# Kernel optimization log

Hardware: AMD Instinct MI355X
Metric: run time of the kernel (lower is better)

## Reference

```python
import jax, jax.numpy as jnp
from jax import lax
import numpy as np

N_POINTS = 2_000_000
EXTENT = 512          # fine voxel extent per axis
STRIDE = 16           # pool kernel/stride
G = EXTENT // STRIDE  # coarse grid per axis = 32
C_IN = 3
C_OUT = 64
K = 3                 # conv kernel size


def setup_inputs() -> dict:
    key = jax.random.key(0)
    k1, k2, k3 = jax.random.split(key, 3)
    coords = jax.random.randint(k1, (N_POINTS, 3), 0, EXTENT, dtype=jnp.int32)
    feats = jax.random.normal(k2, (N_POINTS, C_IN), dtype=jnp.float32)
    # MinkowskiConvolution kernel (no bias by default): [out, in, kD, kH, kW]
    fan_in = C_IN * K ** 3
    W = jax.random.normal(k3, (C_OUT, C_IN, K, K, K), dtype=jnp.float32) / np.sqrt(fan_in)
    return {"coords": coords, "feats": feats, "W": W}


def reference(coords, feats, W):
    # --- MinkowskiAvgPooling(kernel=16, stride=16) ---
    # coarse voxel id per point; average of features of occupied fine voxels in block
    cid = coords // STRIDE                               # [N,3] in [0,G)
    idx = (cid[:, 0] * G + cid[:, 1]) * G + cid[:, 2]    # [N] linearized coarse id
    n_seg = G * G * G
    sums = jax.ops.segment_sum(feats, idx, num_segments=n_seg)               # [G^3,Cin]
    cnt = jax.ops.segment_sum(jnp.ones((feats.shape[0], 1), feats.dtype), idx,
                              num_segments=n_seg)                            # [G^3,1]
    avg = sums / jnp.maximum(cnt, 1.0)                   # zeros at empty coarse voxels

    # --- MinkowskiConvolution(Cin->Cout, k=3, stride=1) on coarse sparse grid ---
    # Empty neighbors contribute zero features, so a dense SAME conv over the
    # zero-filled coarse grid matches the sparse kernel-map gather.
    grid = avg.reshape(1, G, G, G, C_IN).transpose(0, 4, 1, 2, 3)   # NCDHW
    conv = lax.conv_general_dilated(
        grid, W, window_strides=(1, 1, 1), padding="SAME",
        dimension_numbers=("NCDHW", "OIDHW", "NCDHW"))               # [1,Cout,G,G,G]
    # conv outputs only at occupied coarse coords (Minkowski semantics)
    occ = (cnt > 0).astype(conv.dtype).reshape(1, 1, G, G, G)
    conv = conv * occ

    # --- MinkowskiPoolingTranspose(kernel=16, stride=16) ---
    # broadcast each coarse feature back to the occupied fine coords in its block
    flat = conv.transpose(0, 2, 3, 4, 1).reshape(n_seg, C_OUT)       # [G^3,Cout]
    out = flat[idx]                                                  # [N,Cout]
    return out
```

## Files before the change

### kernel.cpp

```cpp
#include <hip/hip_runtime.h>

#define G 32
#define NCELL (G * G * G)
#define C_IN 3
#define C_OUT 64
#define PBLK 64
#define HTHREADS 1024

typedef float f32x4 __attribute__((ext_vector_type(4)));
typedef int   i32x4 __attribute__((ext_vector_type(4)));


__global__ void cellid_kernel(const i32x4* __restrict__ coords4,
                              int* __restrict__ cellid, int n) {
    int t = blockIdx.x * blockDim.x + threadIdx.x;
    int base = t * 4;
    if (base >= n) return;
    i32x4 a = coords4[t * 3 + 0];
    i32x4 b = coords4[t * 3 + 1];
    i32x4 c = coords4[t * 3 + 2];
    int c0 = (((a.x >> 4) * G + (a.y >> 4)) * G + (a.z >> 4));
    int c1 = (((a.w >> 4) * G + (b.x >> 4)) * G + (b.y >> 4));
    int c2 = (((b.z >> 4) * G + (b.w >> 4)) * G + (c.x >> 4));
    int c3 = (((c.y >> 4) * G + (c.z >> 4)) * G + (c.w >> 4));
    if (base + 3 < n) {
        i32x4 r = {c0, c1, c2, c3};
        *(i32x4*)&cellid[base] = r;
    } else {
        cellid[base] = c0;
        if (base + 1 < n) cellid[base + 1] = c1;
        if (base + 2 < n) cellid[base + 2] = c2;
    }
}

__global__ __launch_bounds__(HTHREADS) void histo_kernel(
    const int* __restrict__ cellid,
    const float* __restrict__ feats,
    float* __restrict__ partial,
    int n, int ppc) {
    __shared__ __align__(16) float h[NCELL];
    int vtype = blockIdx.x & 3;
    int chunk = blockIdx.x >> 2;

    f32x4* h4 = (f32x4*)h;
    for (int t = threadIdx.x; t < NCELL / 4; t += HTHREADS)
        h4[t] = (f32x4){0.f, 0.f, 0.f, 0.f};
    __syncthreads();

    int start = chunk * ppc;
    int end = start + ppc; if (end > n) end = n;
    if (vtype < 3) {
        for (int i = start + threadIdx.x; i < end; i += HTHREADS) {
            int c = cellid[i];
            atomicAdd(&h[c], feats[i * 3 + vtype]);
        }
    } else {
        for (int i = start + threadIdx.x; i < end; i += HTHREADS) {
            int c = cellid[i];
            atomicAdd(&h[c], 1.0f);
        }
    }
    __syncthreads();

    f32x4* pp = (f32x4*)(partial + ((size_t)vtype * PBLK + chunk) * NCELL);
    for (int t = threadIdx.x; t < NCELL / 4; t += HTHREADS)
        pp[t] = h4[t];
}

__global__ void reduce_kernel(const float* __restrict__ partial,
                              float* __restrict__ avg) {
    int cell = blockIdx.x * blockDim.x + threadIdx.x;
    if (cell >= NCELL) return;
    float s0 = 0.f, s1 = 0.f, s2 = 0.f, c = 0.f;
    for (int p = 0; p < PBLK; ++p) {
        s0 += partial[((size_t)0 * PBLK + p) * NCELL + cell];
        s1 += partial[((size_t)1 * PBLK + p) * NCELL + cell];
        s2 += partial[((size_t)2 * PBLK + p) * NCELL + cell];
        c  += partial[((size_t)3 * PBLK + p) * NCELL + cell];
    }
    float inv = c > 0.f ? 1.0f / c : 0.f;
    avg[cell * 3 + 0] = s0 * inv;
    avg[cell * 3 + 1] = s1 * inv;
    avg[cell * 3 + 2] = s2 * inv;
}

__global__ void conv_kernel(const float* __restrict__ avg,
                            const float* __restrict__ W,
                            float* __restrict__ convout) {
    __shared__ float wlds[C_OUT * C_IN * 27];
    for (int t = threadIdx.x; t < C_OUT * C_IN * 27; t += blockDim.x)
        wlds[t] = W[t];
    __syncthreads();

    int cell = blockIdx.x * blockDim.x + threadIdx.x;
    if (cell >= NCELL) return;
    int z = cell & 31;
    int y = (cell >> 5) & 31;
    int x = cell >> 10;

    float acc[C_OUT];
#pragma unroll
    for (int c = 0; c < C_OUT; ++c) acc[c] = 0.f;

    for (int kd = 0; kd < 3; ++kd) {
        int nx = x + kd - 1;
        if (nx < 0 || nx >= G) continue;
        for (int kh = 0; kh < 3; ++kh) {
            int ny = y + kh - 1;
            if (ny < 0 || ny >= G) continue;
            for (int kw = 0; kw < 3; ++kw) {
                int nz = z + kw - 1;
                if (nz < 0 || nz >= G) continue;
                int nc = (nx * G + ny) * G + nz;
                float g0 = avg[nc * 3 + 0];
                float g1 = avg[nc * 3 + 1];
                float g2 = avg[nc * 3 + 2];
                int koff = (kd * 3 + kh) * 3 + kw;
#pragma unroll
                for (int co = 0; co < C_OUT; ++co) {
                    const float* wp = &wlds[co * C_IN * 27 + koff];
                    acc[co] += wp[0] * g0 + wp[27] * g1 + wp[54] * g2;
                }
            }
        }
    }
    float* op = &convout[(size_t)cell * C_OUT];
#pragma unroll
    for (int co = 0; co < C_OUT; ++co) op[co] = acc[co];
}

__global__ void gather_kernel(const int* __restrict__ cellid,
                              const f32x4* __restrict__ convout,
                              f32x4* __restrict__ out, int n) {
    long g = (long)blockIdx.x * blockDim.x + threadIdx.x;
    int i = (int)(g >> 4);
    int c4 = (int)(g & 15);
    if (i >= n) return;
    int cell = cellid[i];
    f32x4 val = convout[(size_t)cell * 16 + c4];
    __builtin_nontemporal_store(val, &out[(size_t)i * 16 + c4]);
}

__global__ void scatter_atomic_kernel(const int* __restrict__ coords,
                                      const float* __restrict__ feats,
                                      float* __restrict__ sums,
                                      float* __restrict__ cnt, int n) {
    int i = blockIdx.x * blockDim.x + threadIdx.x;
    if (i >= n) return;
    int x = coords[i * 3 + 0] >> 4;
    int y = coords[i * 3 + 1] >> 4;
    int z = coords[i * 3 + 2] >> 4;
    int cell = (x * G + y) * G + z;
    atomicAdd(&sums[cell * 3 + 0], feats[i * 3 + 0]);
    atomicAdd(&sums[cell * 3 + 1], feats[i * 3 + 1]);
    atomicAdd(&sums[cell * 3 + 2], feats[i * 3 + 2]);
    atomicAdd(&cnt[cell], 1.0f);
}

__global__ void avg_kernel(const float* __restrict__ sums,
                           const float* __restrict__ cnt,
                           float* __restrict__ avg) {
    int cell = blockIdx.x * blockDim.x + threadIdx.x;
    if (cell >= NCELL) return;
    float c = cnt[cell];
    float inv = c > 0.f ? 1.0f / c : 0.f;
    avg[cell * 3 + 0] = sums[cell * 3 + 0] * inv;
    avg[cell * 3 + 1] = sums[cell * 3 + 1] * inv;
    avg[cell * 3 + 2] = sums[cell * 3 + 2] * inv;
}

__global__ void gather_coords_kernel(const int* __restrict__ coords,
                                     const f32x4* __restrict__ convout,
                                     f32x4* __restrict__ out, int n) {
    long g = (long)blockIdx.x * blockDim.x + threadIdx.x;
    int i = (int)(g >> 4);
    int c4 = (int)(g & 15);
    if (i >= n) return;
    int x = coords[i * 3 + 0] >> 4;
    int y = coords[i * 3 + 1] >> 4;
    int z = coords[i * 3 + 2] >> 4;
    int cell = (x * G + y) * G + z;
    out[(size_t)i * 16 + c4] = convout[(size_t)cell * 16 + c4];
}

extern "C" void kernel_launch(void* const* d_in, const int* in_sizes, int n_in,
                              void* d_out, int out_size, void* d_ws, size_t ws_size,
                              hipStream_t stream) {
    const int*   coords = (const int*)d_in[0];
    const float* feats  = (const float*)d_in[1];
    const float* W      = (const float*)d_in[2];
    float* out = (float*)d_out;
    int n = in_sizes[0] / 3;

    float* sums    = (float*)d_ws;
    float* cnt     = sums + NCELL * 3;
    float* avg     = cnt + NCELL;
    float* convout = avg + NCELL * 3;
    int*   cellid  = (int*)(convout + (size_t)NCELL * 64);
    float* partial = (float*)(cellid + ((n + 3) & ~3));

    size_t need = ((size_t)NCELL * (3 + 1 + 3 + 64) + ((n + 3) & ~3) +
                   (size_t)4 * PBLK * NCELL) * 4;
    bool fast = (ws_size >= need);

    long total = (long)n * 16;
    if (fast) {
        int npt4 = (n + 3) / 4;
        cellid_kernel<<<(npt4 + 255) / 256, 256, 0, stream>>>(
            (const i32x4*)coords, cellid, n);
        int ppc = (n + PBLK - 1) / PBLK;
        histo_kernel<<<4 * PBLK, HTHREADS, 0, stream>>>(cellid, feats, partial, n, ppc);
        reduce_kernel<<<NCELL / 256, 256, 0, stream>>>(partial, avg);
        conv_kernel<<<NCELL / 256, 256, 0, stream>>>(avg, W, convout);
        gather_kernel<<<(int)((total + 255) / 256), 256, 0, stream>>>(
            cellid, (const f32x4*)convout, (f32x4*)out, n);
    } else {
        hipMemsetAsync(d_ws, 0, NCELL * 4 * sizeof(float), stream);
        scatter_atomic_kernel<<<(n + 255) / 256, 256, 0, stream>>>(coords, feats, sums, cnt, n);
        avg_kernel<<<NCELL / 256, 256, 0, stream>>>(sums, cnt, avg);
        conv_kernel<<<NCELL / 256, 256, 0, stream>>>(avg, W, convout);
        gather_coords_kernel<<<(int)((total + 255) / 256), 256, 0, stream>>>(
            coords, (const f32x4*)convout, (f32x4*)out, n);
    }
}
```

Measured before the change: 238.2 us.

## Counting-sort points by cell and broadcast conv rows instead of per-point gather

Replaces the per-point gather with a counting sort of point indices by coarse cell: a scan over per-cell counts, per-chunk offsets, and an LDS-atomic scatter build a sorted index list. A broadcast kernel then loads each cell's 64 outputs once and writes them to all its points. Cell ids shrink to 16 bits and histogram blocks are remapped across XCDs. The change removes redundant convout reads but adds several kernels, a single-block scan, and a serial per-cell loop with about 61 points per cell. The broadcast stores are scattered 256-byte rows without nontemporal hints.

```diff
diff --git a/kernel.cpp b/kernel.cpp
--- a/kernel.cpp
+++ b/kernel.cpp
@@ -6,13 +6,15 @@
 #define C_OUT 64
 #define PBLK 64
 #define HTHREADS 1024
-
-typedef float f32x4 __attribute__((ext_vector_type(4)));
-typedef int   i32x4 __attribute__((ext_vector_type(4)));
+#define SCAN_T 1024
+
+typedef float          f32x4  __attribute__((ext_vector_type(4)));
+typedef int            i32x4  __attribute__((ext_vector_type(4)));
+typedef unsigned short u16x4  __attribute__((ext_vector_type(4)));
 
 
 __global__ void cellid_kernel(const i32x4* __restrict__ coords4,
-                              int* __restrict__ cellid, int n) {
+                              unsigned short* __restrict__ cellid, int n) {
     int t = blockIdx.x * blockDim.x + threadIdx.x;
     int base = t * 4;
     if (base >= n) return;
@@ -24,23 +26,26 @@
     int c2 = (((b.z >> 4) * G + (b.w >> 4)) * G + (c.x >> 4));
     int c3 = (((c.y >> 4) * G + (c.z >> 4)) * G + (c.w >> 4));
     if (base + 3 < n) {
-        i32x4 r = {c0, c1, c2, c3};
-        *(i32x4*)&cellid[base] = r;
+        u16x4 r = {(unsigned short)c0, (unsigned short)c1,
+                   (unsigned short)c2, (unsigned short)c3};
+        *(u16x4*)&cellid[base] = r;
     } else {
-        cellid[base] = c0;
-        if (base + 1 < n) cellid[base + 1] = c1;
-        if (base + 2 < n) cellid[base + 2] = c2;
+        cellid[base] = (unsigned short)c0;
+        if (base + 1 < n) cellid[base + 1] = (unsigned short)c1;
+        if (base + 2 < n) cellid[base + 2] = (unsigned short)c2;
     }
 }
 
 __global__ __launch_bounds__(HTHREADS) void histo_kernel(
-    const int* __restrict__ cellid,
+    const unsigned short* __restrict__ cellid,
     const float* __restrict__ feats,
     float* __restrict__ partial,
     int n, int ppc) {
     __shared__ __align__(16) float h[NCELL];
-    int vtype = blockIdx.x & 3;
-    int chunk = blockIdx.x >> 2;
+    int xcd = blockIdx.x & 7;
+    int s   = blockIdx.x >> 3;
+    int chunk = xcd * 8 + (s >> 2);
+    int vtype = s & 3;
 
     f32x4* h4 = (f32x4*)h;
     for (int t = threadIdx.x; t < NCELL / 4; t += HTHREADS)
@@ -68,7 +73,8 @@
 }
 
 __global__ void reduce_kernel(const float* __restrict__ partial,
-                              float* __restrict__ avg) {
+                              float* __restrict__ avg,
+                              int* __restrict__ cnti) {
     int cell = blockIdx.x * blockDim.x + threadIdx.x;
     if (cell >= NCELL) return;
     float s0 = 0.f, s1 = 0.f, s2 = 0.f, c = 0.f;
@@ -82,6 +88,63 @@
     avg[cell * 3 + 0] = s0 * inv;
     avg[cell * 3 + 1] = s1 * inv;
     avg[cell * 3 + 2] = s2 * inv;
+    cnti[cell] = (int)(c + 0.5f);
+}
+
+__global__ __launch_bounds__(SCAN_T) void scan_kernel(
+    const int* __restrict__ cnti, int* __restrict__ cellbase) {
+    __shared__ int ls[SCAN_T];
+    int t = threadIdx.x;
+    const int K = NCELL / SCAN_T;
+    int c0 = t * K;
+    int s = 0;
+#pragma unroll
+    for (int k = 0; k < K; ++k) s += cnti[c0 + k];
+    int val = s;
+    ls[t] = val;
+    __syncthreads();
+    for (int off = 1; off < SCAN_T; off <<= 1) {
+        int other = (t >= off) ? ls[t - off] : 0;
+        __syncthreads();
+        val += other;
+        ls[t] = val;
+        __syncthreads();
+    }
+    int run = val - s;
+    for (int k = 0; k < K; ++k) {
+        cellbase[c0 + k] = run;
+        run += cnti[c0 + k];
+    }
+}
+
+__global__ void chunkoff_kernel(const float* __restrict__ partial,
+                                const int* __restrict__ cellbase,
+                                int* __restrict__ chunkoff) {
+    int c = blockIdx.x * blockDim.x + threadIdx.x;
+    if (c >= NCELL) return;
+    int off = cellbase[c];
+    for (int p = 0; p < PBLK; ++p) {
+        chunkoff[(size_t)p * NCELL + c] = off;
+        off += (int)(partial[((size_t)3 * PBLK + p) * NCELL + c] + 0.5f);
+    }
+}
+
+__global__ __launch_bounds__(HTHREADS) void scatter_idx_kernel(
+    const unsigned short* __restrict__ cellid,
+    const int* __restrict__ chunkoff,
+    int* __restrict__ sortedidx, int n, int ppc) {
+    __shared__ int ctr[NCELL];
+    int p = blockIdx.x;
+    for (int t = threadIdx.x; t < NCELL; t += HTHREADS)
+        ctr[t] = chunkoff[(size_t)p * NCELL + t];
+    __syncthreads();
+    int start = p * ppc;
+    int end = start + ppc; if (end > n) end = n;
+    for (int i = start + threadIdx.x; i < end; i += HTHREADS) {
+        int c = cellid[i];
+        int pos = atomicAdd(&ctr[c], 1);
+        sortedidx[pos] = i;
+    }
 }
 
 __global__ void conv_kernel(const float* __restrict__ avg,
@@ -129,16 +192,21 @@
     for (int co = 0; co < C_OUT; ++co) op[co] = acc[co];
 }
 
-__global__ void gather_kernel(const int* __restrict__ cellid,
-                              const f32x4* __restrict__ convout,
-                              f32x4* __restrict__ out, int n) {
-    long g = (long)blockIdx.x * blockDim.x + threadIdx.x;
-    int i = (int)(g >> 4);
-    int c4 = (int)(g & 15);
-    if (i >= n) return;
-    int cell = cellid[i];
-    f32x4 val = convout[(size_t)cell * 16 + c4];
-    __builtin_nontemporal_store(val, &out[(size_t)i * 16 + c4]);
+__global__ __launch_bounds__(256) void broadcast_kernel(
+    const float* __restrict__ convout,
+    const int* __restrict__ cellbase,
+    const int* __restrict__ cnti,
+    const int* __restrict__ sortedidx,
+    float* __restrict__ out) {
+    int cell = blockIdx.x * 4 + (threadIdx.x >> 6);
+    int lane = threadIdx.x & 63;
+    float v = convout[(size_t)cell * C_OUT + lane];
+    int s = cellbase[cell];
+    int e = s + cnti[cell];
+    for (int j = s; j < e; ++j) {
+        int idx = sortedidx[j];
+        out[(size_t)idx * C_OUT + lane] = v;
+    }
 }
 
 __global__ void scatter_atomic_kernel(const int* __restrict__ coords,
@@ -192,33 +260,43 @@
     float* out = (float*)d_out;
     int n = in_sizes[0] / 3;
 
-    float* sums    = (float*)d_ws;
-    float* cnt     = sums + NCELL * 3;
-    float* avg     = cnt + NCELL;
-    float* convout = avg + NCELL * 3;
-    int*   cellid  = (int*)(convout + (size_t)NCELL * 64);
-    float* partial = (float*)(cellid + ((n + 3) & ~3));
-
-    size_t need = ((size_t)NCELL * (3 + 1 + 3 + 64) + ((n + 3) & ~3) +
-                   (size_t)4 * PBLK * NCELL) * 4;
+    float*          sums      = (float*)d_ws;
+    float*          cnt       = sums + NCELL * 3;
+    float*          avg       = cnt + NCELL;
+    float*          convout   = avg + NCELL * 3;
+    int*            cnti      = (int*)(convout + (size_t)NCELL * 64);
+    int*            cellbase  = cnti + NCELL;
+    int*            chunkoff  = cellbase + NCELL;
+    unsigned short* cellid    = (unsigned short*)(chunkoff + (size_t)PBLK * NCELL);
+    size_t          cid_elems = ((size_t)n + 7) & ~(size_t)7;
+    int*            sortedidx = (int*)(cellid + cid_elems);
+    float*          partial   = (float*)(sortedidx + cid_elems);
+
+    size_t need = (size_t)NCELL * (3 + 1 + 3 + 64 + 1 + 1 + PBLK) * 4 +
+                  cid_elems * 2 + cid_elems * 4 +
+                  (size_t)4 * PBLK * NCELL * 4;
     bool fast = (ws_size >= need);
 
-    long total = (long)n * 16;
     if (fast) {
         int npt4 = (n + 3) / 4;
         cellid_kernel<<<(npt4 + 255) / 256, 256, 0, stream>>>(
             (const i32x4*)coords, cellid, n);
         int ppc = (n + PBLK - 1) / PBLK;
         histo_kernel<<<4 * PBLK, HTHREADS, 0, stream>>>(cellid, feats, partial, n, ppc);
-        reduce_kernel<<<NCELL / 256, 256, 0, stream>>>(partial, avg);
+        reduce_kernel<<<NCELL / 256, 256, 0, stream>>>(partial, avg, cnti);
+        scan_kernel<<<1, SCAN_T, 0, stream>>>(cnti, cellbase);
+        chunkoff_kernel<<<NCELL / 256, 256, 0, stream>>>(partial, cellbase, chunkoff);
+        scatter_idx_kernel<<<PBLK, HTHREADS, 0, stream>>>(cellid, chunkoff,
+                                                          sortedidx, n, ppc);
         conv_kernel<<<NCELL / 256, 256, 0, stream>>>(avg, W, convout);
-        gather_kernel<<<(int)((total + 255) / 256), 256, 0, stream>>>(
-            cellid, (const f32x4*)convout, (f32x4*)out, n);
+        broadcast_kernel<<<NCELL / 4, 256, 0, stream>>>(convout, cellbase, cnti,
+                                                        sortedidx, out);
     } else {
         hipMemsetAsync(d_ws, 0, NCELL * 4 * sizeof(float), stream);
         scatter_atomic_kernel<<<(n + 255) / 256, 256, 0, stream>>>(coords, feats, sums, cnt, n);
         avg_kernel<<<NCELL / 256, 256, 0, stream>>>(sums, cnt, avg);
         conv_kernel<<<NCELL / 256, 256, 0, stream>>>(avg, W, convout);
+        long total = (long)n * 16;
         gather_coords_kernel<<<(int)((total + 255) / 256), 256, 0, stream>>>(
             coords, (const f32x4*)convout, (f32x4*)out, n);
     }
```

Result: slower. 284.6 us (+19.5%).

## Shrink cell ids to u16, remap histogram blocks per XCD, stage gather through LDS

Applied to the files above, without the earlier changes.

Cell ids are stored as 16-bit values, which halves the traffic for writing and re-reading them in the histogram and gather kernels. Histogram blocks are renumbered so that the chunk and channel blocks sharing a chunk are grouped by blockIdx mod 8, aiming for better L2 locality across XCDs. The gather becomes a persistent kernel with a fixed grid that stages each 256-point tile in LDS before streaming out. The staging adds two barriers per tile, and the smaller fixed grid may leave the gather less able to hide memory latency.

```diff
diff --git a/kernel.cpp b/kernel.cpp
--- a/kernel.cpp
+++ b/kernel.cpp
@@ -6,13 +6,17 @@
 #define C_OUT 64
 #define PBLK 64
 #define HTHREADS 1024
-
-typedef float f32x4 __attribute__((ext_vector_type(4)));
-typedef int   i32x4 __attribute__((ext_vector_type(4)));
+#define GT 256
+#define GTILE 256
+#define GBLOCKS 512
+
+typedef float          f32x4  __attribute__((ext_vector_type(4)));
+typedef int            i32x4  __attribute__((ext_vector_type(4)));
+typedef unsigned short u16x4  __attribute__((ext_vector_type(4)));
 
 
 __global__ void cellid_kernel(const i32x4* __restrict__ coords4,
-                              int* __restrict__ cellid, int n) {
+                              unsigned short* __restrict__ cellid, int n) {
     int t = blockIdx.x * blockDim.x + threadIdx.x;
     int base = t * 4;
     if (base >= n) return;
@@ -24,23 +28,26 @@
     int c2 = (((b.z >> 4) * G + (b.w >> 4)) * G + (c.x >> 4));
     int c3 = (((c.y >> 4) * G + (c.z >> 4)) * G + (c.w >> 4));
     if (base + 3 < n) {
-        i32x4 r = {c0, c1, c2, c3};
-        *(i32x4*)&cellid[base] = r;
+        u16x4 r = {(unsigned short)c0, (unsigned short)c1,
+                   (unsigned short)c2, (unsigned short)c3};
+        *(u16x4*)&cellid[base] = r;
     } else {
-        cellid[base] = c0;
-        if (base + 1 < n) cellid[base + 1] = c1;
-        if (base + 2 < n) cellid[base + 2] = c2;
+        cellid[base] = (unsigned short)c0;
+        if (base + 1 < n) cellid[base + 1] = (unsigned short)c1;
+        if (base + 2 < n) cellid[base + 2] = (unsigned short)c2;
     }
 }
 
 __global__ __launch_bounds__(HTHREADS) void histo_kernel(
-    const int* __restrict__ cellid,
+    const unsigned short* __restrict__ cellid,
     const float* __restrict__ feats,
     float* __restrict__ partial,
     int n, int ppc) {
     __shared__ __align__(16) float h[NCELL];
-    int vtype = blockIdx.x & 3;
-    int chunk = blockIdx.x >> 2;
+    int xcd = blockIdx.x & 7;
+    int s   = blockIdx.x >> 3;
+    int chunk = xcd * 8 + (s >> 2);
+    int vtype = s & 3;
 
     f32x4* h4 = (f32x4*)h;
     for (int t = threadIdx.x; t < NCELL / 4; t += HTHREADS)
@@ -129,16 +136,28 @@
     for (int co = 0; co < C_OUT; ++co) op[co] = acc[co];
 }
 
-__global__ void gather_kernel(const int* __restrict__ cellid,
-                              const f32x4* __restrict__ convout,
-                              f32x4* __restrict__ out, int n) {
-    long g = (long)blockIdx.x * blockDim.x + threadIdx.x;
-    int i = (int)(g >> 4);
-    int c4 = (int)(g & 15);
-    if (i >= n) return;
-    int cell = cellid[i];
-    f32x4 val = convout[(size_t)cell * 16 + c4];
-    __builtin_nontemporal_store(val, &out[(size_t)i * 16 + c4]);
+__global__ __launch_bounds__(GT) void gather_lds_kernel(
+    const unsigned short* __restrict__ cellid,
+    const f32x4* __restrict__ tab,
+    f32x4* __restrict__ out, int n) {
+    __shared__ f32x4 buf[GTILE * 16];
+    int ntiles = (n + GTILE - 1) / GTILE;
+    for (int t = blockIdx.x; t < ntiles; t += GBLOCKS) {
+        int base = t * GTILE;
+        int cnt = min(GTILE, n - base);
+        int tasks = cnt * 16;
+        __syncthreads();
+        for (int k = threadIdx.x; k < tasks; k += GT) {
+            int p  = k >> 4;
+            int c4 = k & 15;
+            int cell = cellid[base + p];
+            buf[k] = tab[(size_t)cell * 16 + c4];
+        }
+        __syncthreads();
+        f32x4* dst = &out[(size_t)base * 16];
+        for (int k = threadIdx.x; k < tasks; k += GT)
+            __builtin_nontemporal_store(buf[k], &dst[k]);
+    }
 }
 
 __global__ void scatter_atomic_kernel(const int* __restrict__ coords,
@@ -192,18 +211,18 @@
     float* out = (float*)d_out;
     int n = in_sizes[0] / 3;
 
-    float* sums    = (float*)d_ws;
-    float* cnt     = sums + NCELL * 3;
-    float* avg     = cnt + NCELL;
-    float* convout = avg + NCELL * 3;
-    int*   cellid  = (int*)(convout + (size_t)NCELL * 64);
-    float* partial = (float*)(cellid + ((n + 3) & ~3));
-
-    size_t need = ((size_t)NCELL * (3 + 1 + 3 + 64) + ((n + 3) & ~3) +
-                   (size_t)4 * PBLK * NCELL) * 4;
+    float*          sums      = (float*)d_ws;
+    float*          cnt       = sums + NCELL * 3;
+    float*          avg       = cnt + NCELL;
+    float*          convout   = avg + NCELL * 3;
+    unsigned short* cellid    = (unsigned short*)(convout + (size_t)NCELL * 64);
+    size_t          cid_elems = ((size_t)n + 7) & ~(size_t)7;
+    float*          partial   = (float*)(cellid + cid_elems);
+
+    size_t need = (size_t)NCELL * (3 + 1 + 3 + 64) * 4 + cid_elems * 2 +
+                  (size_t)4 * PBLK * NCELL * 4;
     bool fast = (ws_size >= need);
 
-    long total = (long)n * 16;
     if (fast) {
         int npt4 = (n + 3) / 4;
         cellid_kernel<<<(npt4 + 255) / 256, 256, 0, stream>>>(
@@ -212,13 +231,14 @@
         histo_kernel<<<4 * PBLK, HTHREADS, 0, stream>>>(cellid, feats, partial, n, ppc);
         reduce_kernel<<<NCELL / 256, 256, 0, stream>>>(partial, avg);
         conv_kernel<<<NCELL / 256, 256, 0, stream>>>(avg, W, convout);
-        gather_kernel<<<(int)((total + 255) / 256), 256, 0, stream>>>(
+        gather_lds_kernel<<<GBLOCKS, GT, 0, stream>>>(
             cellid, (const f32x4*)convout, (f32x4*)out, n);
     } else {
         hipMemsetAsync(d_ws, 0, NCELL * 4 * sizeof(float), stream);
         scatter_atomic_kernel<<<(n + 255) / 256, 256, 0, stream>>>(coords, feats, sums, cnt, n);
         avg_kernel<<<NCELL / 256, 256, 0, stream>>>(sums, cnt, avg);
         conv_kernel<<<NCELL / 256, 256, 0, stream>>>(avg, W, convout);
+        long total = (long)n * 16;
         gather_coords_kernel<<<(int)((total + 255) / 256), 256, 0, stream>>>(
             coords, (const f32x4*)convout, (f32x4*)out, n);
     }
```

After: 301.1 us. 1.26x slower.
